# Kernel optimization log

Measured on AMD Instinct MI355X. Metric: run time of the kernel, lower is better.

## Reference

```python
import jax, jax.numpy as jnp
import numpy as np

B, F, S, D = 256, 8, 200, 64
H = 36  # hidden units per field
EPS = 1e-3  # Dice BN epsilon


def setup_inputs() -> dict:
    key0 = jax.random.key(0)
    ks = jax.random.split(key0, 8)
    query = jax.random.normal(ks[0], (B, F, D), dtype=jnp.float32)
    key = jax.random.normal(ks[1], (B, F, S, D), dtype=jnp.float32)
    sequence_num = jax.random.randint(ks[2], (B, F), 1, S + 1, dtype=jnp.int32)
    W_h = jax.random.normal(ks[3], (F, 3 * D, H), dtype=jnp.float32) * 0.05
    b_h = jnp.zeros((F, H), dtype=jnp.float32)
    alpha = jnp.zeros((F,), dtype=jnp.float32)
    W_o = jax.random.normal(ks[4], (F, H, 1), dtype=jnp.float32) * 0.05
    b_o = jnp.zeros((F, 1), dtype=jnp.float32)
    return {"query": query, "key": key, "W_h": W_h, "b_h": b_h,
            "alpha": alpha, "W_o": W_o, "b_o": b_o,
            "sequence_num": sequence_num, "training": 1}


def reference(query, key, W_h, b_h, alpha, W_o, b_o, sequence_num, training):
    # query: [B,F,D], key: [B,F,S,D]
    q = query[:, :, None, :]                      # broadcast instead of tile
    qb = jnp.broadcast_to(q, key.shape)           # [B,F,S,D]
    cat = jnp.concatenate([key, qb, q - key], axis=-1)  # [B,F,S,3D]
    # per-field Dense(36), vectorized across fields
    h = jnp.einsum('bfsc,fch->bfsh', cat, W_h) + b_h[None, :, None, :]
    # Dice: BatchNorm (no affine, training-mode batch stats over batch+seq per field/feature)
    mean = h.mean(axis=(0, 2), keepdims=True)
    var = h.var(axis=(0, 2), keepdims=True)
    p = jax.nn.sigmoid((h - mean) * jax.lax.rsqrt(var + EPS))
    h = (alpha[None, :, None, None] * (1.0 - p) + p) * h
    # per-field Dense(1) -> attention scores [B,F,S]
    scores = jnp.einsum('bfsh,fh->bfs', h, W_o[:, :, 0]) + b_o[None, :, 0, None]
    # mask invalid positions and softmax over sequence
    mask = jnp.arange(key.shape[2])[None, None, :] < sequence_num[:, :, None]
    scores = jnp.where(mask, scores, -jnp.inf)
    attn = jax.nn.softmax(scores, axis=-1)        # [B,F,S]
    # weighted sum over sequence -> [B,F,D]
    return jnp.einsum('bfs,bfsd->bfd', attn, key)
```

## Files before the change

### kernel.cpp

```cpp
#include <hip/hip_runtime.h>
#include <math.h>

#define NB 256
#define NF 8
#define NS 200
#define ND 64
#define NH 36
#define EPSV 1e-3f
#define LDA 72
#define MT 13

typedef __attribute__((ext_vector_type(8))) short short8;
typedef __attribute__((ext_vector_type(4))) short short4v;
typedef __attribute__((ext_vector_type(4))) float f32x4;

__device__ __forceinline__ unsigned short f32_to_bf16(float x) {
    unsigned u = __float_as_uint(x);
    unsigned r = u + 0x7FFFu + ((u >> 16) & 1u);
    return (unsigned short)(r >> 16);
}
__device__ __forceinline__ float bf16_to_f32(unsigned short h) {
    return __uint_as_float(((unsigned)h) << 16);
}

template <bool STATS>
__global__ __launch_bounds__(256, 2) void k_main(
    const float* __restrict__ query, const float* __restrict__ key,
    const float* __restrict__ W_h, const float* __restrict__ b_h,
    const float* __restrict__ alpha, const float* __restrict__ W_o,
    const float* __restrict__ b_o, const int* __restrict__ seqn,
    float* __restrict__ ws, float* __restrict__ out)
{
    __shared__ __align__(16) unsigned short Ahi[208 * LDA];
    __shared__ __align__(16) unsigned short Alo[208 * LDA];
    __shared__ __align__(16) unsigned short Bt[48 * LDA];
    __shared__ float qrow[64];
    __shared__ float qt_s[48];
    __shared__ float meanP[48], invP[48], woP[48];
    __shared__ float sumP[48], sqP[48];
    __shared__ float scores[NS];
    __shared__ float warr[NS];
    __shared__ float red[256];
    __shared__ float pout[4][64];

    const int blk = blockIdx.x;
    const int f = blk & (NF - 1);
    const int b = blk >> 3;
    const int tid = threadIdx.x;
    const int lane = tid & 63;
    const int wv = tid >> 6;

    const float* Wf = W_h + (size_t)f * (3 * ND * NH);
    const float* kbase = key + (size_t)(b * NF + f) * (NS * ND);

    if (tid < 64) qrow[tid] = query[(size_t)(b * NF + f) * ND + tid];
    if (tid >= 64 && tid < 112) {
        int h = tid - 64;
        if (STATS) { sumP[h] = 0.f; sqP[h] = 0.f; }
        else if (h < NH) {
            meanP[h] = ws[576 + f * NH + h];
            invP[h]  = ws[864 + f * NH + h];
            woP[h]   = W_o[f * NH + h];
        } else { meanP[h] = 0.f; invP[h] = 0.f; woP[h] = 0.f; }
    }
    for (int i = tid; i < 48 * 64; i += 256) {
        int h = i >> 6, d = i & 63;
        float v = (h < NH) ? (Wf[d * NH + h] - Wf[(2 * ND + d) * NH + h]) : 0.f;
        Bt[h * LDA + d] = f32_to_bf16(v);
    }
    __syncthreads();

    {
        const float4* kb4 = (const float4*)kbase;
        const int c = tid & 15;
        const int r0 = tid >> 4;
        float4 kv[MT];
        #pragma unroll
        for (int i = 0; i < MT; ++i) {
            int sr = r0 + 16 * i;
            kv[i] = (sr < NS) ? kb4[sr * 16 + c] : make_float4(0.f, 0.f, 0.f, 0.f);
        }
        #pragma unroll
        for (int i = 0; i < MT; ++i) {
            int sr = r0 + 16 * i;
            float vs[4] = {kv[i].x, kv[i].y, kv[i].z, kv[i].w};
            short4v h4, l4;
            #pragma unroll
            for (int j = 0; j < 4; ++j) {
                unsigned short hb = f32_to_bf16(vs[j]);
                float rem = vs[j] - bf16_to_f32(hb);
                h4[j] = (short)hb;
                l4[j] = (short)f32_to_bf16(rem);
            }
            *(short4v*)&Ahi[sr * LDA + 4 * c] = h4;
            *(short4v*)&Alo[sr * LDA + 4 * c] = l4;
        }
    }
    if (tid < 48) {
        float acc = 0.f;
        if (tid < NH) {
            acc = b_h[f * NH + tid];
            for (int d = 0; d < ND; ++d)
                acc += qrow[d] * (Wf[(ND + d) * NH + tid] + Wf[(2 * ND + d) * NH + tid]);
        }
        qt_s[tid] = acc;
    }
    __syncthreads();

    const int col = lane & 15;
    const int quad = lane >> 4;
    const float alf = STATS ? 0.f : alpha[f];
    const float bo  = STATS ? 0.f : b_o[f];

    short8 bf[3][2];
    #pragma unroll
    for (int nt = 0; nt < 3; ++nt)
        #pragma unroll
        for (int ks = 0; ks < 2; ++ks)
            bf[nt][ks] = *(const short8*)&Bt[(nt * 16 + col) * LDA + ks * 32 + quad * 8];

    float s_sum[3] = {0.f, 0.f, 0.f}, s_sq[3] = {0.f, 0.f, 0.f};

    for (int mt = wv; mt < MT; mt += 4) {
        const int abase = (mt * 16 + col) * LDA + quad * 8;
        short8 ah0 = *(const short8*)&Ahi[abase];
        short8 ah1 = *(const short8*)&Ahi[abase + 32];
        short8 al0 = *(const short8*)&Alo[abase];
        short8 al1 = *(const short8*)&Alo[abase + 32];
        float part[4] = {0.f, 0.f, 0.f, 0.f};
        #pragma unroll
        for (int nt = 0; nt < 3; ++nt) {
            float qv = qt_s[nt * 16 + col];
            f32x4 acc = {qv, qv, qv, qv};
            acc = __builtin_amdgcn_mfma_f32_16x16x32_bf16(ah0, bf[nt][0], acc, 0, 0, 0);
            acc = __builtin_amdgcn_mfma_f32_16x16x32_bf16(ah1, bf[nt][1], acc, 0, 0, 0);
            acc = __builtin_amdgcn_mfma_f32_16x16x32_bf16(al0, bf[nt][0], acc, 0, 0, 0);
            acc = __builtin_amdgcn_mfma_f32_16x16x32_bf16(al1, bf[nt][1], acc, 0, 0, 0);
            if (STATS) {
                #pragma unroll
                for (int r = 0; r < 4; ++r) {
                    int s = mt * 16 + quad * 4 + r;
                    float v = (s < NS) ? acc[r] : 0.f;
                    s_sum[nt] += v;
                    s_sq[nt]  += v * v;
                }
            } else {
                float mn = meanP[nt * 16 + col], iv = invP[nt * 16 + col], wo = woP[nt * 16 + col];
                #pragma unroll
                for (int r = 0; r < 4; ++r) {
                    float h = acc[r];
                    float p = 1.f / (1.f + __expf(-(h - mn) * iv));
                    part[r] += (alf + (1.f - alf) * p) * h * wo;
                }
            }
        }
        if (!STATS) {
            #pragma unroll
            for (int r = 0; r < 4; ++r) {
                float v = part[r];
                v += __shfl_xor(v, 1, 64);
                v += __shfl_xor(v, 2, 64);
                v += __shfl_xor(v, 4, 64);
                v += __shfl_xor(v, 8, 64);
                if (col == 0) {
                    int s = mt * 16 + quad * 4 + r;
                    if (s < NS) scores[s] = v + bo;
                }
            }
        }
    }

    if (STATS) {
        #pragma unroll
        for (int nt = 0; nt < 3; ++nt) {
            float sv = s_sum[nt], qv = s_sq[nt];
            sv += __shfl_xor(sv, 16, 64); sv += __shfl_xor(sv, 32, 64);
            qv += __shfl_xor(qv, 16, 64); qv += __shfl_xor(qv, 32, 64);
            if (quad == 0 && wv == (nt & 3)) {  }
            if (quad == 0) {
                atomicAdd(&sumP[nt * 16 + col], sv);
                atomicAdd(&sqP[nt * 16 + col], qv);
            }
        }
        __syncthreads();
        if (tid < NH) {
            atomicAdd(&ws[f * NH + tid], sumP[tid]);
            atomicAdd(&ws[288 + f * NH + tid], sqP[tid]);
        }
        return;
    }

    __syncthreads();
    const int sq_n = seqn[b * NF + f];
    const bool val = (tid < NS) && (tid < sq_n);
    float sval = val ? scores[tid] : -1e30f;
    red[tid] = sval;
    __syncthreads();
    for (int st = 128; st >= 1; st >>= 1) {
        if (tid < st) red[tid] = fmaxf(red[tid], red[tid + st]);
        __syncthreads();
    }
    const float maxv = red[0];
    __syncthreads();
    float e = val ? __expf(sval - maxv) : 0.f;
    red[tid] = e;
    __syncthreads();
    for (int st = 128; st >= 1; st >>= 1) {
        if (tid < st) red[tid] += red[tid + st];
        __syncthreads();
    }
    const float isum = 1.f / red[0];
    if (tid < NS) warr[tid] = e * isum;
    __syncthreads();

    {
        const int d = lane;
        float acc = 0.f;
        for (int s = wv * 50; s < wv * 50 + 50; ++s) {
            float kvf = bf16_to_f32(Ahi[s * LDA + d]) + bf16_to_f32(Alo[s * LDA + d]);
            acc += warr[s] * kvf;
        }
        pout[wv][d] = acc;
    }
    __syncthreads();
    if (tid < 64)
        out[(size_t)(b * NF + f) * ND + tid] =
            pout[0][tid] + pout[1][tid] + pout[2][tid] + pout[3][tid];
}

__global__ void k_finalize(float* __restrict__ ws) {
    const int t = blockIdx.x * blockDim.x + threadIdx.x;
    if (t < NF * NH) {
        const float inv_n = 1.f / (float)(NB * NS);
        const float m   = ws[t] * inv_n;
        const float var = ws[288 + t] * inv_n - m * m;
        ws[576 + t] = m;
        ws[864 + t] = rsqrtf(var + EPSV);
    }
}

extern "C" void kernel_launch(void* const* d_in, const int* in_sizes, int n_in,
                              void* d_out, int out_size, void* d_ws, size_t ws_size,
                              hipStream_t stream) {
    const float* query = (const float*)d_in[0];
    const float* key   = (const float*)d_in[1];
    const float* W_h   = (const float*)d_in[2];
    const float* b_h   = (const float*)d_in[3];
    const float* alpha = (const float*)d_in[4];
    const float* W_o   = (const float*)d_in[5];
    const float* b_o   = (const float*)d_in[6];
    const int*   seqn  = (const int*)d_in[7];
    float* out = (float*)d_out;
    float* ws  = (float*)d_ws;

    hipMemsetAsync(ws, 0, 576 * sizeof(float), stream);
    k_main<true><<<NB * NF, 256, 0, stream>>>(query, key, W_h, b_h, alpha, W_o, b_o, seqn, ws, out);
    k_finalize<<<1, 512, 0, stream>>>(ws);
    k_main<false><<<NB * NF, 256, 0, stream>>>(query, key, W_h, b_h, alpha, W_o, b_o, seqn, ws, out);
}
```

Before: 250.1 us.

## Split into prep/stats/attn kernels, drop bf16 hi/lo split, keep keys in registers

Adds a prep kernel that computes the per-row query term and the bf16 weight tiles once into the workspace, instead of recomputing them in every block. The stats and attention kernels now load keys straight from global memory into registers as single bf16 operands, dropping the hi/lo split and the LDS staging. This halves the MFMA work. The attention kernel merges the finalize step, uses wave-shuffle softmax reductions, and reuses the register bf16 keys for the weighted sum. The cost is lower precision: keys are bf16-rounded both in the scores and in the output sum, which may change results beyond tolerance.

```diff
diff --git a/kernel.cpp b/kernel.cpp
--- a/kernel.cpp
+++ b/kernel.cpp
@@ -6,12 +6,15 @@
 #define NS 200
 #define ND 64
 #define NH 36
+#define MT 13
 #define EPSV 1e-3f
-#define LDA 72
-#define MT 13
+
+#define WS_SUM 0
+#define WS_SQ  288
+#define WS_QT  1152
+#define WS_WK  (1152 + 2048 * 48)
 
 typedef __attribute__((ext_vector_type(8))) short short8;
-typedef __attribute__((ext_vector_type(4))) short short4v;
 typedef __attribute__((ext_vector_type(4))) float f32x4;
 
 __device__ __forceinline__ unsigned short f32_to_bf16(float x) {
@@ -22,139 +25,181 @@
 __device__ __forceinline__ float bf16_to_f32(unsigned short h) {
     return __uint_as_float(((unsigned)h) << 16);
 }
-
-template <bool STATS>
-__global__ __launch_bounds__(256, 2) void k_main(
-    const float* __restrict__ query, const float* __restrict__ key,
-    const float* __restrict__ W_h, const float* __restrict__ b_h,
-    const float* __restrict__ alpha, const float* __restrict__ W_o,
-    const float* __restrict__ b_o, const int* __restrict__ seqn,
-    float* __restrict__ ws, float* __restrict__ out)
+__device__ __forceinline__ short8 cvt8(float4 a, float4 b) {
+    short8 r;
+    r[0] = (short)f32_to_bf16(a.x); r[1] = (short)f32_to_bf16(a.y);
+    r[2] = (short)f32_to_bf16(a.z); r[3] = (short)f32_to_bf16(a.w);
+    r[4] = (short)f32_to_bf16(b.x); r[5] = (short)f32_to_bf16(b.y);
+    r[6] = (short)f32_to_bf16(b.z); r[7] = (short)f32_to_bf16(b.w);
+    return r;
+}
+
+__global__ __launch_bounds__(256) void k_prep(
+    const float* __restrict__ query, const float* __restrict__ W_h,
+    const float* __restrict__ b_h, float* __restrict__ ws)
 {
-    __shared__ __align__(16) unsigned short Ahi[208 * LDA];
-    __shared__ __align__(16) unsigned short Alo[208 * LDA];
-    __shared__ __align__(16) unsigned short Bt[48 * LDA];
-    __shared__ float qrow[64];
-    __shared__ float qt_s[48];
-    __shared__ float meanP[48], invP[48], woP[48];
-    __shared__ float sumP[48], sqP[48];
-    __shared__ float scores[NS];
-    __shared__ float warr[NS];
-    __shared__ float red[256];
-    __shared__ float pout[4][64];
-
+    const int blk = blockIdx.x, tid = threadIdx.x;
+    if (blk < NB) {
+        __shared__ float qs[NF * ND];
+        for (int i = tid; i < NF * ND; i += 256)
+            qs[i] = query[(size_t)blk * NF * ND + i];
+        __syncthreads();
+        for (int i = tid; i < NF * 48; i += 256) {
+            int f = i / 48, h = i - f * 48;
+            float acc = 0.f;
+            if (h < NH) {
+                const float* Wf = W_h + (size_t)f * (3 * ND * NH);
+                acc = b_h[f * NH + h];
+                for (int d = 0; d < ND; ++d)
+                    acc += qs[f * ND + d] * (Wf[(ND + d) * NH + h] + Wf[(2 * ND + d) * NH + h]);
+            }
+            ws[WS_QT + (size_t)(blk * NF + f) * 48 + h] = acc;
+        }
+    } else {
+        const int f = blk - NB;
+        const float* Wf = W_h + (size_t)f * (3 * ND * NH);
+        unsigned short* wk = (unsigned short*)(ws + WS_WK) + f * (48 * ND);
+        for (int i = tid; i < 48 * ND; i += 256) {
+            int h = i >> 6, d = i & 63;
+            float v = (h < NH) ? (Wf[d * NH + h] - Wf[(2 * ND + d) * NH + h]) : 0.f;
+            wk[h * ND + d] = f32_to_bf16(v);
+        }
+    }
+}
+
+__global__ __launch_bounds__(256, 4) void k_stats(
+    const float* __restrict__ key, float* __restrict__ ws)
+{
     const int blk = blockIdx.x;
     const int f = blk & (NF - 1);
-    const int b = blk >> 3;
     const int tid = threadIdx.x;
     const int lane = tid & 63;
     const int wv = tid >> 6;
-
-    const float* Wf = W_h + (size_t)f * (3 * ND * NH);
-    const float* kbase = key + (size_t)(b * NF + f) * (NS * ND);
-
-    if (tid < 64) qrow[tid] = query[(size_t)(b * NF + f) * ND + tid];
-    if (tid >= 64 && tid < 112) {
-        int h = tid - 64;
-        if (STATS) { sumP[h] = 0.f; sqP[h] = 0.f; }
-        else if (h < NH) {
-            meanP[h] = ws[576 + f * NH + h];
-            invP[h]  = ws[864 + f * NH + h];
-            woP[h]   = W_o[f * NH + h];
-        } else { meanP[h] = 0.f; invP[h] = 0.f; woP[h] = 0.f; }
-    }
-    for (int i = tid; i < 48 * 64; i += 256) {
-        int h = i >> 6, d = i & 63;
-        float v = (h < NH) ? (Wf[d * NH + h] - Wf[(2 * ND + d) * NH + h]) : 0.f;
-        Bt[h * LDA + d] = f32_to_bf16(v);
-    }
-    __syncthreads();
-
-    {
-        const float4* kb4 = (const float4*)kbase;
-        const int c = tid & 15;
-        const int r0 = tid >> 4;
-        float4 kv[MT];
-        #pragma unroll
-        for (int i = 0; i < MT; ++i) {
-            int sr = r0 + 16 * i;
-            kv[i] = (sr < NS) ? kb4[sr * 16 + c] : make_float4(0.f, 0.f, 0.f, 0.f);
-        }
-        #pragma unroll
-        for (int i = 0; i < MT; ++i) {
-            int sr = r0 + 16 * i;
-            float vs[4] = {kv[i].x, kv[i].y, kv[i].z, kv[i].w};
-            short4v h4, l4;
-            #pragma unroll
-            for (int j = 0; j < 4; ++j) {
-                unsigned short hb = f32_to_bf16(vs[j]);
-                float rem = vs[j] - bf16_to_f32(hb);
-                h4[j] = (short)hb;
-                l4[j] = (short)f32_to_bf16(rem);
-            }
-            *(short4v*)&Ahi[sr * LDA + 4 * c] = h4;
-            *(short4v*)&Alo[sr * LDA + 4 * c] = l4;
-        }
-    }
-    if (tid < 48) {
-        float acc = 0.f;
-        if (tid < NH) {
-            acc = b_h[f * NH + tid];
-            for (int d = 0; d < ND; ++d)
-                acc += qrow[d] * (Wf[(ND + d) * NH + tid] + Wf[(2 * ND + d) * NH + tid]);
-        }
-        qt_s[tid] = acc;
-    }
-    __syncthreads();
-
     const int col = lane & 15;
     const int quad = lane >> 4;
-    const float alf = STATS ? 0.f : alpha[f];
-    const float bo  = STATS ? 0.f : b_o[f];
-
-    short8 bf[3][2];
-    #pragma unroll
-    for (int nt = 0; nt < 3; ++nt)
+
+    __shared__ float sumP[48], sqP[48];
+    if (tid < 48) { sumP[tid] = 0.f; sqP[tid] = 0.f; }
+    __syncthreads();
+
+    const float* kbase = key + (size_t)blk * (NS * ND);
+    const unsigned short* wk = (const unsigned short*)(ws + WS_WK) + f * (48 * ND);
+
+    short8 bfr[3][2];
+    float qv[3];
+    #pragma unroll
+    for (int nt = 0; nt < 3; ++nt) {
         #pragma unroll
         for (int ks = 0; ks < 2; ++ks)
-            bf[nt][ks] = *(const short8*)&Bt[(nt * 16 + col) * LDA + ks * 32 + quad * 8];
+            bfr[nt][ks] = *(const short8*)&wk[(nt * 16 + col) * ND + ks * 32 + quad * 8];
+        qv[nt] = ws[WS_QT + (size_t)blk * 48 + nt * 16 + col];
+    }
 
     float s_sum[3] = {0.f, 0.f, 0.f}, s_sq[3] = {0.f, 0.f, 0.f};
-
     for (int mt = wv; mt < MT; mt += 4) {
-        const int abase = (mt * 16 + col) * LDA + quad * 8;
-        short8 ah0 = *(const short8*)&Ahi[abase];
-        short8 ah1 = *(const short8*)&Ahi[abase + 32];
-        short8 al0 = *(const short8*)&Alo[abase];
-        short8 al1 = *(const short8*)&Alo[abase + 32];
-        float part[4] = {0.f, 0.f, 0.f, 0.f};
+        const int s = 16 * mt + col;
+        const float4* p = (const float4*)(kbase + (size_t)(s < NS ? s : NS - 1) * ND + quad * 8);
+        float4 a0 = p[0], a1 = p[1];
+        float4 b0 = p[8], b1 = p[9];
+        short8 ah0 = cvt8(a0, a1);
+        short8 ah1 = cvt8(b0, b1);
         #pragma unroll
         for (int nt = 0; nt < 3; ++nt) {
-            float qv = qt_s[nt * 16 + col];
-            f32x4 acc = {qv, qv, qv, qv};
-            acc = __builtin_amdgcn_mfma_f32_16x16x32_bf16(ah0, bf[nt][0], acc, 0, 0, 0);
-            acc = __builtin_amdgcn_mfma_f32_16x16x32_bf16(ah1, bf[nt][1], acc, 0, 0, 0);
-            acc = __builtin_amdgcn_mfma_f32_16x16x32_bf16(al0, bf[nt][0], acc, 0, 0, 0);
-            acc = __builtin_amdgcn_mfma_f32_16x16x32_bf16(al1, bf[nt][1], acc, 0, 0, 0);
-            if (STATS) {
+            f32x4 acc = {qv[nt], qv[nt], qv[nt], qv[nt]};
+            acc = __builtin_amdgcn_mfma_f32_16x16x32_bf16(ah0, bfr[nt][0], acc, 0, 0, 0);
+            acc = __builtin_amdgcn_mfma_f32_16x16x32_bf16(ah1, bfr[nt][1], acc, 0, 0, 0);
+            #pragma unroll
+            for (int r = 0; r < 4; ++r) {
+                int srow = 16 * mt + quad * 4 + r;
+                if (srow < NS) { float v = acc[r]; s_sum[nt] += v; s_sq[nt] += v * v; }
+            }
+        }
+    }
+    #pragma unroll
+    for (int nt = 0; nt < 3; ++nt) {
+        float sv = s_sum[nt], qq = s_sq[nt];
+        sv += __shfl_xor(sv, 16, 64); sv += __shfl_xor(sv, 32, 64);
+        qq += __shfl_xor(qq, 16, 64); qq += __shfl_xor(qq, 32, 64);
+        if (quad == 0) {
+            atomicAdd(&sumP[nt * 16 + col], sv);
+            atomicAdd(&sqP[nt * 16 + col], qq);
+        }
+    }
+    __syncthreads();
+    if (tid < NH) {
+        atomicAdd(&ws[WS_SUM + f * NH + tid], sumP[tid]);
+        atomicAdd(&ws[WS_SQ + f * NH + tid], sqP[tid]);
+    }
+}
+
+__global__ __launch_bounds__(256, 3) void k_attn(
+    const float* __restrict__ key, const float* __restrict__ alpha,
+    const float* __restrict__ W_o, const float* __restrict__ b_o,
+    const int* __restrict__ seqn, const float* __restrict__ ws,
+    float* __restrict__ out)
+{
+    const int blk = blockIdx.x;
+    const int f = blk & (NF - 1);
+    const int tid = threadIdx.x;
+    const int lane = tid & 63;
+    const int wv = tid >> 6;
+    const int col = lane & 15;
+    const int quad = lane >> 4;
+
+    __shared__ float sw[208];
+    __shared__ float redM[4], redS[4];
+    __shared__ float pout[4][64];
+
+    const float* kbase = key + (size_t)blk * (NS * ND);
+    const unsigned short* wk = (const unsigned short*)(ws + WS_WK) + f * (48 * ND);
+    const float inv_n = 1.f / (float)(NB * NS);
+
+    short8 bfr[3][2];
+    float qv[3], mn[3], iv[3], wo[3];
+    #pragma unroll
+    for (int nt = 0; nt < 3; ++nt) {
+        #pragma unroll
+        for (int ks = 0; ks < 2; ++ks)
+            bfr[nt][ks] = *(const short8*)&wk[(nt * 16 + col) * ND + ks * 32 + quad * 8];
+        const int hh = nt * 16 + col;
+        const bool hv = hh < NH;
+        const int hc = hv ? hh : 0;
+        qv[nt] = ws[WS_QT + (size_t)blk * 48 + hh];
+        const float sm = ws[WS_SUM + f * NH + hc];
+        const float sq = ws[WS_SQ + f * NH + hc];
+        const float m = sm * inv_n;
+        mn[nt] = m;
+        iv[nt] = rsqrtf(fmaxf(sq * inv_n - m * m, 0.f) + EPSV);
+        wo[nt] = hv ? W_o[f * NH + hh] : 0.f;
+    }
+    const float alf = alpha[f];
+    const float bo = b_o[f];
+    const int sq_n = seqn[blk];
+
+    short8 kah[4][2];
+    #pragma unroll
+    for (int t = 0; t < 4; ++t) {
+        const int mt = wv + 4 * t;
+        if (mt < MT) {
+            const int s = 16 * mt + col;
+            const float4* p = (const float4*)(kbase + (size_t)(s < NS ? s : NS - 1) * ND + quad * 8);
+            float4 a0 = p[0], a1 = p[1];
+            float4 b0 = p[8], b1 = p[9];
+            kah[t][0] = cvt8(a0, a1);
+            kah[t][1] = cvt8(b0, b1);
+            float part[4] = {0.f, 0.f, 0.f, 0.f};
+            #pragma unroll
+            for (int nt = 0; nt < 3; ++nt) {
+                f32x4 acc = {qv[nt], qv[nt], qv[nt], qv[nt]};
+                acc = __builtin_amdgcn_mfma_f32_16x16x32_bf16(kah[t][0], bfr[nt][0], acc, 0, 0, 0);
+                acc = __builtin_amdgcn_mfma_f32_16x16x32_bf16(kah[t][1], bfr[nt][1], acc, 0, 0, 0);
                 #pragma unroll
                 for (int r = 0; r < 4; ++r) {
-                    int s = mt * 16 + quad * 4 + r;
-                    float v = (s < NS) ? acc[r] : 0.f;
-                    s_sum[nt] += v;
-                    s_sq[nt]  += v * v;
+                    const float h = acc[r];
+                    const float pg = 1.f / (1.f + __expf(-(h - mn[nt]) * iv[nt]));
+                    part[r] += (alf + (1.f - alf) * pg) * h * wo[nt];
                 }
-            } else {
-                float mn = meanP[nt * 16 + col], iv = invP[nt * 16 + col], wo = woP[nt * 16 + col];
-                #pragma unroll
-                for (int r = 0; r < 4; ++r) {
-                    float h = acc[r];
-                    float p = 1.f / (1.f + __expf(-(h - mn) * iv));
-                    part[r] += (alf + (1.f - alf) * p) * h * wo;
-                }
-            }
-        }
-        if (!STATS) {
+            }
             #pragma unroll
             for (int r = 0; r < 4; ++r) {
                 float v = part[r];
@@ -162,81 +207,65 @@
                 v += __shfl_xor(v, 2, 64);
                 v += __shfl_xor(v, 4, 64);
                 v += __shfl_xor(v, 8, 64);
-                if (col == 0) {
-                    int s = mt * 16 + quad * 4 + r;
-                    if (s < NS) scores[s] = v + bo;
-                }
-            }
-        }
-    }
-
-    if (STATS) {
-        #pragma unroll
-        for (int nt = 0; nt < 3; ++nt) {
-            float sv = s_sum[nt], qv = s_sq[nt];
-            sv += __shfl_xor(sv, 16, 64); sv += __shfl_xor(sv, 32, 64);
-            qv += __shfl_xor(qv, 16, 64); qv += __shfl_xor(qv, 32, 64);
-            if (quad == 0 && wv == (nt & 3)) {  }
-            if (quad == 0) {
-                atomicAdd(&sumP[nt * 16 + col], sv);
-                atomicAdd(&sqP[nt * 16 + col], qv);
-            }
-        }
-        __syncthreads();
-        if (tid < NH) {
-            atomicAdd(&ws[f * NH + tid], sumP[tid]);
-            atomicAdd(&ws[288 + f * NH + tid], sqP[tid]);
-        }
-        return;
-    }
-
-    __syncthreads();
-    const int sq_n = seqn[b * NF + f];
-    const bool val = (tid < NS) && (tid < sq_n);
-    float sval = val ? scores[tid] : -1e30f;
-    red[tid] = sval;
-    __syncthreads();
-    for (int st = 128; st >= 1; st >>= 1) {
-        if (tid < st) red[tid] = fmaxf(red[tid], red[tid + st]);
-        __syncthreads();
-    }
-    const float maxv = red[0];
-    __syncthreads();
-    float e = val ? __expf(sval - maxv) : 0.f;
-    red[tid] = e;
-    __syncthreads();
-    for (int st = 128; st >= 1; st >>= 1) {
-        if (tid < st) red[tid] += red[tid + st];
-        __syncthreads();
-    }
-    const float isum = 1.f / red[0];
-    if (tid < NS) warr[tid] = e * isum;
-    __syncthreads();
-
-    {
-        const int d = lane;
-        float acc = 0.f;
-        for (int s = wv * 50; s < wv * 50 + 50; ++s) {
-            float kvf = bf16_to_f32(Ahi[s * LDA + d]) + bf16_to_f32(Alo[s * LDA + d]);
-            acc += warr[s] * kvf;
-        }
-        pout[wv][d] = acc;
+                const int srow = 16 * mt + quad * 4 + r;
+                if (col == 0 && srow < NS) sw[srow] = v + bo;
+            }
+        }
+    }
+    __syncthreads();
+
+    const bool valid = (tid < 208) && (tid < sq_n);
+    const float sc = valid ? sw[tid] : -1e30f;
+    float m = sc;
+    m = fmaxf(m, __shfl_xor(m, 1, 64));  m = fmaxf(m, __shfl_xor(m, 2, 64));
+    m = fmaxf(m, __shfl_xor(m, 4, 64));  m = fmaxf(m, __shfl_xor(m, 8, 64));
+    m = fmaxf(m, __shfl_xor(m, 16, 64)); m = fmaxf(m, __shfl_xor(m, 32, 64));
+    if (lane == 0) redM[wv] = m;
+    __syncthreads();
+    const float maxv = fmaxf(fmaxf(redM[0], redM[1]), fmaxf(redM[2], redM[3]));
+    const float e = valid ? __expf(sc - maxv) : 0.f;
+    float l = e;
+    l += __shfl_xor(l, 1, 64);  l += __shfl_xor(l, 2, 64);
+    l += __shfl_xor(l, 4, 64);  l += __shfl_xor(l, 8, 64);
+    l += __shfl_xor(l, 16, 64); l += __shfl_xor(l, 32, 64);
+    if (lane == 0) redS[wv] = l;
+    __syncthreads();
+    const float isum = 1.f / (redS[0] + redS[1] + redS[2] + redS[3]);
+    if (tid < 208) sw[tid] = e * isum;
+    __syncthreads();
+
+    float po0[8] = {0,0,0,0,0,0,0,0}, po1[8] = {0,0,0,0,0,0,0,0};
+    #pragma unroll
+    for (int t = 0; t < 4; ++t) {
+        const int mt = wv + 4 * t;
+        if (mt < MT) {
+            const float w = sw[16 * mt + col];
+            #pragma unroll
+            for (int j = 0; j < 8; ++j) {
+                po0[j] += w * bf16_to_f32((unsigned short)kah[t][0][j]);
+                po1[j] += w * bf16_to_f32((unsigned short)kah[t][1][j]);
+            }
+        }
+    }
+    #pragma unroll
+    for (int off = 1; off <= 8; off <<= 1) {
+        #pragma unroll
+        for (int j = 0; j < 8; ++j) {
+            po0[j] += __shfl_xor(po0[j], off, 64);
+            po1[j] += __shfl_xor(po1[j], off, 64);
+        }
+    }
+    if (col == 0) {
+        #pragma unroll
+        for (int j = 0; j < 8; ++j) {
+            pout[wv][quad * 8 + j] = po0[j];
+            pout[wv][32 + quad * 8 + j] = po1[j];
+        }
     }
     __syncthreads();
     if (tid < 64)
-        out[(size_t)(b * NF + f) * ND + tid] =
+        out[(size_t)blk * ND + tid] =
             pout[0][tid] + pout[1][tid] + pout[2][tid] + pout[3][tid];
-}
-
-__global__ void k_finalize(float* __restrict__ ws) {
-    const int t = blockIdx.x * blockDim.x + threadIdx.x;
-    if (t < NF * NH) {
-        const float inv_n = 1.f / (float)(NB * NS);
-        const float m   = ws[t] * inv_n;
-        const float var = ws[288 + t] * inv_n - m * m;
-        ws[576 + t] = m;
-        ws[864 + t] = rsqrtf(var + EPSV);
-    }
 }
 
 extern "C" void kernel_launch(void* const* d_in, const int* in_sizes, int n_in,
@@ -254,7 +283,7 @@
     float* ws  = (float*)d_ws;
 
     hipMemsetAsync(ws, 0, 576 * sizeof(float), stream);
-    k_main<true><<<NB * NF, 256, 0, stream>>>(query, key, W_h, b_h, alpha, W_o, b_o, seqn, ws, out);
-    k_finalize<<<1, 512, 0, stream>>>(ws);
-    k_main<false><<<NB * NF, 256, 0, stream>>>(query, key, W_h, b_h, alpha, W_o, b_o, seqn, ws, out);
-}
+    k_prep<<<NB + NF, 256, 0, stream>>>(query, W_h, b_h, ws);
+    k_stats<<<NB * NF, 256, 0, stream>>>(key, ws);
+    k_attn<<<NB * NF, 256, 0, stream>>>(key, alpha, W_o, b_o, seqn, ws, out);
+}
```

After: 213.1 us. 14.8% less time.
